# Performance work log

Measured on AMD Instinct MI355X. Metric: run time of the kernel, lower is better.

## Reference

```python
import jax, jax.numpy as jnp
import numpy as np
import math

N_EXP = 8
TOP_K = 2
CAPACITY_FACTOR = 1.25


def _capacity(num_tokens):
    cap = math.floor(TOP_K * CAPACITY_FACTOR * num_tokens / N_EXP)
    cap += cap % 2  # round up to even, as in nanoMoE
    return int(cap)


def setup_inputs() -> dict:
    key = jax.random.key(0)
    k1, k2, k3, k4 = jax.random.split(key, 4)
    B, C, d = 4, 1024, 1024
    x = jax.random.normal(k1, (B, C, d), dtype=jnp.float32)
    w_g = jax.random.normal(k2, (d, N_EXP), dtype=jnp.float32) * 0.02
    c_fc = jax.random.normal(k3, (N_EXP, d, 4 * d), dtype=jnp.float32) * 0.02
    c_proj = jax.random.normal(k4, (N_EXP, 4 * d, d), dtype=jnp.float32) * 0.02
    return {"x": x, "w_g": w_g, "c_fc": c_fc, "c_proj": c_proj}


def reference(x, w_g, c_fc, c_proj):
    B, C, d = x.shape
    T = B * C  # num_tokens (static)
    cap = _capacity(T)
    xt = x.reshape(T, d)

    # ---- Router (no noise: use_noisy_top_k=False, eval) ----
    logits = xt @ w_g                                   # [T, n_exp]
    top_v, top_i = jax.lax.top_k(logits, TOP_K)         # [T, k]
    full = jnp.full_like(logits, -jnp.inf)
    full = full.at[jnp.arange(T)[:, None], top_i].set(top_v)
    probs = jax.nn.softmax(full, axis=-1)               # [T, n_exp]

    # expert assignment mask and intra-expert rank (capacity dropping)
    exp_mask = jax.nn.one_hot(top_i, N_EXP, dtype=jnp.int32)       # [T, k, n_exp]
    exp_mask = jnp.transpose(exp_mask, (1, 0, 2))                  # [k, T, n_exp]
    exp_rank = jnp.cumsum(exp_mask.reshape(TOP_K * T, N_EXP), axis=0) - 1
    exp_rank = exp_rank.reshape(TOP_K, T, N_EXP)
    exp_mask = exp_mask * (exp_rank < cap).astype(jnp.int32)       # drop overflow
    exp_rank = jnp.sum(exp_mask * exp_rank, axis=-1)               # [k, T] slot id

    exp_weights = exp_mask.astype(x.dtype) * probs[None]           # [k, T, n_exp]
    rank_oh = jax.nn.one_hot(exp_rank, cap, dtype=x.dtype)         # [k, T, cap]
    # dense combine weights [T, n_exp, cap] (as in original code)
    cb_weight = jnp.einsum('kte,ktc->tec', exp_weights, rank_oh)
    sec_mask = (cb_weight != 0).astype(x.dtype)                    # dispatch mask

    # dispatch tokens into per-expert batches [n_exp, cap, d]
    exp_batches = jnp.einsum('tec,td->ecd', sec_mask, xt)

    # ---- MLPExperts: batched GEMM -> GELU (exact) -> batched GEMM ----
    h = jax.nn.gelu(jnp.einsum('ecd,edf->ecf', exp_batches, c_fc), approximate=False)
    exp_out = jnp.einsum('ecf,efd->ecd', h, c_proj)                # [n_exp, cap, d]

    # ---- weighted combine: [T, n_exp*cap] @ [n_exp*cap, d] ----
    out = cb_weight.reshape(T, N_EXP * cap) @ exp_out.reshape(N_EXP * cap, d)
    return out.reshape(B, C, d)
```

## Files before the change

### kernel.cpp

```cpp
#include <hip/hip_runtime.h>
#include <hip/hip_bf16.h>
#include <math.h>

#define T_TOK 4096
#define D     1024
#define DFF   4096
#define NEXP  8
#define CAP   1280
#define TOPK  2

typedef __bf16 bf16x8 __attribute__((ext_vector_type(8)));
typedef float floatx4 __attribute__((ext_vector_type(4)));

__device__ __forceinline__ unsigned short f2bf(float f) {
  union { float f; unsigned u; } un; un.f = f;
  unsigned r = un.u + 0x7FFF + ((un.u >> 16) & 1);
  return (unsigned short)(r >> 16);
}

__global__ __launch_bounds__(256) void router_kernel(
    const float* __restrict__ x, const float* __restrict__ wg,
    int* __restrict__ top_e, float* __restrict__ top_p) {
  int t = blockIdx.x * 4 + (threadIdx.x >> 6);
  int lane = threadIdx.x & 63;
  if (t >= T_TOK) return;
  const float* xr = x + (size_t)t * D;
  float acc[NEXP];
#pragma unroll
  for (int e = 0; e < NEXP; e++) acc[e] = 0.f;
  for (int dd = lane; dd < D; dd += 64) {
    float xv = xr[dd];
    const float* wr = wg + dd * NEXP;
#pragma unroll
    for (int e = 0; e < NEXP; e++) acc[e] += xv * wr[e];
  }
#pragma unroll
  for (int off = 32; off > 0; off >>= 1) {
#pragma unroll
    for (int e = 0; e < NEXP; e++) acc[e] += __shfl_xor(acc[e], off, 64);
  }
  if (lane == 0) {
    int b0 = 0; float v0 = acc[0];
    for (int e = 1; e < NEXP; e++) if (acc[e] > v0) { v0 = acc[e]; b0 = e; }
    int b1 = -1; float v1 = -INFINITY;
    for (int e = 0; e < NEXP; e++) if (e != b0 && acc[e] > v1) { v1 = acc[e]; b1 = e; }
    float e1 = expf(v1 - v0);
    float s = 1.0f + e1;
    top_e[t * 2 + 0] = b0; top_e[t * 2 + 1] = b1;
    top_p[t * 2 + 0] = 1.0f / s; top_p[t * 2 + 1] = e1 / s;
  }
}

__global__ __launch_bounds__(1024) void rank_kernel(
    const int* __restrict__ top_e, const float* __restrict__ top_p,
    int* __restrict__ slot_token, int* __restrict__ tok_slot,
    float* __restrict__ tok_w) {
  __shared__ int wsum[16][NEXP];
  __shared__ int wscan[16][NEXP];
  int tid = threadIdx.x;
  int lane = tid & 63, w = tid >> 6;

  for (int s = tid; s < NEXP * CAP; s += 1024) slot_token[s] = -1;
  __syncthreads();

  int base[NEXP];
#pragma unroll
  for (int e = 0; e < NEXP; e++) base[e] = 0;

  for (int k = 0; k < TOPK; k++) {
    int cnt[NEXP];
#pragma unroll
    for (int e = 0; e < NEXP; e++) cnt[e] = 0;
    int eloc[4];
#pragma unroll
    for (int i = 0; i < 4; i++) {
      int t = tid * 4 + i;
      int e = top_e[t * 2 + k];
      eloc[i] = e;
#pragma unroll
      for (int q = 0; q < NEXP; q++) cnt[q] += (q == e);
    }
    int inc[NEXP];
#pragma unroll
    for (int e = 0; e < NEXP; e++) inc[e] = cnt[e];
    for (int off = 1; off < 64; off <<= 1) {
#pragma unroll
      for (int e = 0; e < NEXP; e++) {
        int v = __shfl_up(inc[e], off, 64);
        if (lane >= off) inc[e] += v;
      }
    }
    if (lane == 63)
#pragma unroll
      for (int e = 0; e < NEXP; e++) wsum[w][e] = inc[e];
    __syncthreads();
    if (w == 0 && lane < 16) {
      int s[NEXP];
#pragma unroll
      for (int e = 0; e < NEXP; e++) s[e] = wsum[lane][e];
      for (int off = 1; off < 16; off <<= 1) {
#pragma unroll
        for (int e = 0; e < NEXP; e++) {
          int v = __shfl_up(s[e], off, 64);
          if (lane >= off) s[e] += v;
        }
      }
#pragma unroll
      for (int e = 0; e < NEXP; e++) wscan[lane][e] = s[e];
    }
    __syncthreads();
    int excl[NEXP];
#pragma unroll
    for (int e = 0; e < NEXP; e++)
      excl[e] = inc[e] - cnt[e] + (w ? wscan[w - 1][e] : 0) + base[e];

    int run[NEXP];
#pragma unroll
    for (int e = 0; e < NEXP; e++) run[e] = 0;
#pragma unroll
    for (int i = 0; i < 4; i++) {
      int t = tid * 4 + i;
      int e = eloc[i];
      int r = 0;
#pragma unroll
      for (int q = 0; q < NEXP; q++)
        if (q == e) { r = excl[q] + run[q]; run[q]++; }
      if (r < CAP) {
        slot_token[e * CAP + r] = t;
        tok_slot[t * 2 + k] = e * CAP + r;
      } else {
        tok_slot[t * 2 + k] = -1;
      }
      tok_w[t * 2 + k] = top_p[t * 2 + k];
    }
#pragma unroll
    for (int e = 0; e < NEXP; e++) base[e] += wscan[15][e];
    __syncthreads();
  }
}

__global__ __launch_bounds__(256) void gather_cvt_kernel(
    const float* __restrict__ x, const int* __restrict__ slot_token,
    unsigned short* __restrict__ xb) {
  int slot = blockIdx.x;
  int tok = slot_token[slot];
  int i = threadIdx.x;
  float4 v = make_float4(0.f, 0.f, 0.f, 0.f);
  if (tok >= 0) v = ((const float4*)(x + (size_t)tok * D))[i];
  ushort4 o;
  o.x = f2bf(v.x); o.y = f2bf(v.y); o.z = f2bf(v.z); o.w = f2bf(v.w);
  ((ushort4*)(xb + (size_t)slot * D))[i] = o;
}

__global__ __launch_bounds__(256) void transpose_cvt_kernel(
    const float* __restrict__ src, unsigned short* __restrict__ dst,
    int R, int Cc) {
  __shared__ float tile[64][65];
  int e = blockIdx.z;
  src += (size_t)e * R * Cc;
  dst += (size_t)e * R * Cc;
  int r0 = blockIdx.y * 64, c0 = blockIdx.x * 64;
  int tr = threadIdx.x >> 4;
  int tc = (threadIdx.x & 15) * 4;
#pragma unroll
  for (int i = 0; i < 64; i += 16) {
    float4 v = *(const float4*)(src + (size_t)(r0 + tr + i) * Cc + c0 + tc);
    tile[tr + i][tc + 0] = v.x;
    tile[tr + i][tc + 1] = v.y;
    tile[tr + i][tc + 2] = v.z;
    tile[tr + i][tc + 3] = v.w;
  }
  __syncthreads();
#pragma unroll
  for (int i = 0; i < 64; i += 16) {
    int c = tr + i, r = tc;
    ushort4 o;
    o.x = f2bf(tile[r + 0][c]);
    o.y = f2bf(tile[r + 1][c]);
    o.z = f2bf(tile[r + 2][c]);
    o.w = f2bf(tile[r + 3][c]);
    *(ushort4*)(dst + (size_t)(c0 + c) * R + r0 + r) = o;
  }
}

template <int MODE>
__global__ __launch_bounds__(512, 2) void gemm8_kernel(
    const unsigned short* __restrict__ A,
    const unsigned short* __restrict__ Bt,
    void* __restrict__ Cv) {
  constexpr int NN   = (MODE == 0) ? DFF : D;
  constexpr int KK   = (MODE == 0) ? D : DFF;
  constexpr int NTN  = NN / 256;
  constexpr int NKT  = KK / 64;
  constexpr int STOT = NKT * 4;
  constexpr int REG  = 256 * 32;

  __shared__ unsigned short As[4 * REG];
  __shared__ unsigned short Bs[4 * REG];

  int e    = blockIdx.x & 7;
  int idx  = blockIdx.x >> 3;
  int row0 = (idx / NTN) * 256;
  int col0 = (idx % NTN) * 256;

  int tid  = threadIdx.x;
  int lane = tid & 63, wave = tid >> 6;
  int wm = wave >> 2, wn = wave & 3;
  int fr = lane & 15, fq = lane >> 4;
  int lanesw = (fq ^ ((fr >> 1) & 3)) * 8;

  int srow  = tid >> 2;
  int lslot = (tid & 3) ^ ((srow >> 1) & 3);
  const unsigned short* asrc =
      A + (size_t)e * CAP * KK + (size_t)(row0 + srow) * KK + lslot * 8;
  const unsigned short* bsrc =
      Bt + (size_t)e * NN * KK + (size_t)(col0 + srow) * KK + lslot * 8;

  floatx4 acc[8][4];
#pragma unroll
  for (int m = 0; m < 8; m++)
#pragma unroll
    for (int n = 0; n < 4; n++) acc[m][n] = (floatx4){0.f, 0.f, 0.f, 0.f};

  auto stage = [&](int s) {
    if (s >= STOT) return;
    int kt = s >> 2, j = s & 3, hh = j >> 1;
    const unsigned short* src = (j & 1) ? bsrc : asrc;
    unsigned short* dst =
        ((j & 1) ? Bs : As) + ((kt & 1) * 2 + hh) * REG + tid * 8;
    size_t go = (size_t)kt * 64 + hh * 32;
    __builtin_amdgcn_global_load_lds(
        (const __attribute__((address_space(1))) unsigned int*)(src + go),
        (__attribute__((address_space(3))) unsigned int*)dst, 16, 0, 0);
    __builtin_amdgcn_global_load_lds(
        (const __attribute__((address_space(1))) unsigned int*)(src + go +
                                                               (size_t)128 * KK),
        (__attribute__((address_space(3))) unsigned int*)(dst + REG / 2), 16, 0,
        0);
  };

#pragma unroll
  for (int s = 0; s < 6; s++) stage(s);

  bf16x8 aq[4], bq[4];

  for (int kt = 0; kt < NKT; kt++) {
    const unsigned short* a0 = As + (kt & 1) * 2 * REG;
    const unsigned short* b0 = Bs + (kt & 1) * 2 * REG;
    const unsigned short* a1 = a0 + REG;
    const unsigned short* b1 = b0 + REG;
    int abase = (wm * 128 + fr) * 32 + lanesw;
    int bbase = (wn * 64 + fr) * 32 + lanesw;

    stage(kt * 4 + 6);
    if (kt == NKT - 1)
      asm volatile("s_waitcnt vmcnt(0)" ::: "memory");
    else
      asm volatile("s_waitcnt vmcnt(6)" ::: "memory");
    __builtin_amdgcn_s_barrier();
    __builtin_amdgcn_sched_barrier(0);
#pragma unroll
    for (int n = 0; n < 4; n++)
      bq[n] = *(const bf16x8*)&b0[bbase + n * 512];
#pragma unroll
    for (int m = 0; m < 4; m++)
      aq[m] = *(const bf16x8*)&a0[abase + m * 512];
    __builtin_amdgcn_s_setprio(1);
#pragma unroll
    for (int m = 0; m < 4; m++)
#pragma unroll
      for (int n = 0; n < 4; n++)
        acc[m][n] = __builtin_amdgcn_mfma_f32_16x16x32_bf16(aq[m], bq[n],
                                                            acc[m][n], 0, 0, 0);
    __builtin_amdgcn_s_setprio(0);
    __builtin_amdgcn_s_barrier();

#pragma unroll
    for (int m = 0; m < 4; m++)
      aq[m] = *(const bf16x8*)&a0[abase + 2048 + m * 512];
    stage(kt * 4 + 7);
    __builtin_amdgcn_s_barrier();
    __builtin_amdgcn_s_setprio(1);
#pragma unroll
    for (int m = 0; m < 4; m++)
#pragma unroll
      for (int n = 0; n < 4; n++)
        acc[4 + m][n] = __builtin_amdgcn_mfma_f32_16x16x32_bf16(
            aq[m], bq[n], acc[4 + m][n], 0, 0, 0);
    __builtin_amdgcn_s_setprio(0);
    __builtin_amdgcn_s_barrier();

#pragma unroll
    for (int n = 0; n < 4; n++)
      bq[n] = *(const bf16x8*)&b1[bbase + n * 512];
#pragma unroll
    for (int m = 0; m < 4; m++)
      aq[m] = *(const bf16x8*)&a1[abase + m * 512];
    stage(kt * 4 + 8);
    __builtin_amdgcn_s_barrier();
    __builtin_amdgcn_s_setprio(1);
#pragma unroll
    for (int m = 0; m < 4; m++)
#pragma unroll
      for (int n = 0; n < 4; n++)
        acc[m][n] = __builtin_amdgcn_mfma_f32_16x16x32_bf16(aq[m], bq[n],
                                                            acc[m][n], 0, 0, 0);
    __builtin_amdgcn_s_setprio(0);
    __builtin_amdgcn_s_barrier();

#pragma unroll
    for (int m = 0; m < 4; m++)
      aq[m] = *(const bf16x8*)&a1[abase + 2048 + m * 512];
    stage(kt * 4 + 9);
    __builtin_amdgcn_s_barrier();
    __builtin_amdgcn_s_setprio(1);
#pragma unroll
    for (int m = 0; m < 4; m++)
#pragma unroll
      for (int n = 0; n < 4; n++)
        acc[4 + m][n] = __builtin_amdgcn_mfma_f32_16x16x32_bf16(
            aq[m], bq[n], acc[4 + m][n], 0, 0, 0);
    __builtin_amdgcn_s_setprio(0);
    __builtin_amdgcn_s_barrier();
  }

  if (MODE == 0) {
    unsigned short* Ce = (unsigned short*)Cv + (size_t)e * CAP * DFF +
                         (size_t)(row0 + wm * 128 + fq * 4) * DFF + col0 +
                         wn * 64 + fr;
#pragma unroll
    for (int m = 0; m < 8; m++)
#pragma unroll
      for (int r = 0; r < 4; r++) {
        size_t ro = (size_t)(m * 16 + r) * DFF;
#pragma unroll
        for (int n = 0; n < 4; n++) {
          float v = acc[m][n][r];
          v = 0.5f * v * (1.f + erff(v * 0.70710678118654752f));
          Ce[ro + n * 16] = f2bf(v);
        }
      }
  } else {
    float* Ce = (float*)Cv + (size_t)e * CAP * D +
                (size_t)(row0 + wm * 128 + fq * 4) * D + col0 + wn * 64 + fr;
#pragma unroll
    for (int m = 0; m < 8; m++)
#pragma unroll
      for (int r = 0; r < 4; r++) {
        size_t ro = (size_t)(m * 16 + r) * D;
#pragma unroll
        for (int n = 0; n < 4; n++) Ce[ro + n * 16] = acc[m][n][r];
      }
  }
}

__global__ __launch_bounds__(256) void combine_kernel(
    const float* __restrict__ eo, const int* __restrict__ tok_slot,
    const float* __restrict__ tok_w, float* __restrict__ out) {
  int t = blockIdx.x;
  int i = threadIdx.x;
  float4 acc = make_float4(0.f, 0.f, 0.f, 0.f);
#pragma unroll
  for (int k = 0; k < TOPK; k++) {
    int s = tok_slot[t * 2 + k];
    if (s >= 0) {
      float w = tok_w[t * 2 + k];
      float4 v = ((const float4*)(eo + (size_t)s * D))[i];
      acc.x += w * v.x;
      acc.y += w * v.y;
      acc.z += w * v.z;
      acc.w += w * v.w;
    }
  }
  ((float4*)(out + (size_t)t * D))[i] = acc;
}

extern "C" void kernel_launch(void* const* d_in, const int* in_sizes, int n_in,
                              void* d_out, int out_size, void* d_ws, size_t ws_size,
                              hipStream_t stream) {
  const float* x     = (const float*)d_in[0];
  const float* wg    = (const float*)d_in[1];
  const float* cfc   = (const float*)d_in[2];
  const float* cproj = (const float*)d_in[3];
  float* out = (float*)d_out;

  char* ws = (char*)d_ws;
  size_t off = 0;
  auto alloc = [&](size_t bytes) -> void* {
    void* p = ws + off;
    off += (bytes + 255) & ~(size_t)255;
    return p;
  };
  int*   top_e      = (int*)  alloc((size_t)T_TOK * 2 * 4);
  float* top_p      = (float*)alloc((size_t)T_TOK * 2 * 4);
  int*   slot_token = (int*)  alloc((size_t)NEXP * CAP * 4);
  int*   tok_slot   = (int*)  alloc((size_t)T_TOK * 2 * 4);
  float* tok_w      = (float*)alloc((size_t)T_TOK * 2 * 4);
  unsigned short* xb      = (unsigned short*)alloc((size_t)NEXP * CAP * D * 2);
  unsigned short* cfc_t   = (unsigned short*)alloc((size_t)NEXP * D * DFF * 2);
  unsigned short* cproj_t = (unsigned short*)alloc((size_t)NEXP * DFF * D * 2);
  unsigned short* h       = (unsigned short*)alloc((size_t)NEXP * CAP * DFF * 2);
  float* eo = (float*)xb;

  transpose_cvt_kernel<<<dim3(DFF / 64, D / 64, NEXP), 256, 0, stream>>>(
      cfc, cfc_t, D, DFF);
  transpose_cvt_kernel<<<dim3(D / 64, DFF / 64, NEXP), 256, 0, stream>>>(
      cproj, cproj_t, DFF, D);

  router_kernel<<<T_TOK / 4, 256, 0, stream>>>(x, wg, top_e, top_p);
  rank_kernel<<<1, 1024, 0, stream>>>(top_e, top_p, slot_token, tok_slot, tok_w);
  gather_cvt_kernel<<<NEXP * CAP, 256, 0, stream>>>(x, slot_token, xb);

  gemm8_kernel<0><<<NEXP * (CAP / 256) * (DFF / 256), 512, 0, stream>>>(
      xb, cfc_t, h);
  gemm8_kernel<1><<<NEXP * (CAP / 256) * (D / 256), 512, 0, stream>>>(
      h, cproj_t, eo);

  combine_kernel<<<T_TOK, 256, 0, stream>>>(eo, tok_slot, tok_w, out);
}
```

Measured before the change: 617.2 us.

## Reschedule GEMM LDS reads ahead of barriers and use fast erf GELU

Moves the LDS fragment reads ahead of the stage issue and barrier, so the vmcnt wait happens once per K iteration at the end instead of at the start. Explicit lgkmcnt waits and sched_barriers keep register loads overlapped with in-flight global-to-LDS copies. Also replaces erff in the GELU epilogue with an Abramowitz-Stegun polynomial built on rcp and exp, trading a small accuracy loss for fewer instructions. The waitcnt rework risks race conditions if the counts are wrong.

Result: faster. 604.3 us (-2.1%).

```diff
diff --git a/kernel.cpp b/kernel.cpp
--- a/kernel.cpp
+++ b/kernel.cpp
@@ -16,6 +16,17 @@
   union { float f; unsigned u; } un; un.f = f;
   unsigned r = un.u + 0x7FFF + ((un.u >> 16) & 1);
   return (unsigned short)(r >> 16);
+}
+
+__device__ __forceinline__ float gelu_exact(float v) {
+  float z  = v * 0.70710678118654752f;
+  float az = fabsf(z);
+  float t  = __builtin_amdgcn_rcpf(fmaf(0.3275911f, az, 1.0f));
+  float p  = fmaf(fmaf(fmaf(fmaf(1.061405429f, t, -1.453152027f), t,
+                            1.421413741f), t, -0.284496736f), t, 0.254829592f) * t;
+  float ex = __expf(-z * z);
+  float er = copysignf(fmaf(-p, ex, 1.0f), z);
+  return 0.5f * v * (1.0f + er);
 }
 
 __global__ __launch_bounds__(256) void router_kernel(
@@ -241,6 +252,8 @@
 
 #pragma unroll
   for (int s = 0; s < 6; s++) stage(s);
+  asm volatile("s_waitcnt vmcnt(4)" ::: "memory");
+  __builtin_amdgcn_s_barrier();
 
   bf16x8 aq[4], bq[4];
 
@@ -252,19 +265,15 @@
     int abase = (wm * 128 + fr) * 32 + lanesw;
     int bbase = (wn * 64 + fr) * 32 + lanesw;
 
+#pragma unroll
+    for (int n = 0; n < 4; n++) bq[n] = *(const bf16x8*)&b0[bbase + n * 512];
+#pragma unroll
+    for (int m = 0; m < 4; m++) aq[m] = *(const bf16x8*)&a0[abase + m * 512];
     stage(kt * 4 + 6);
-    if (kt == NKT - 1)
-      asm volatile("s_waitcnt vmcnt(0)" ::: "memory");
-    else
-      asm volatile("s_waitcnt vmcnt(6)" ::: "memory");
-    __builtin_amdgcn_s_barrier();
-    __builtin_amdgcn_sched_barrier(0);
-#pragma unroll
-    for (int n = 0; n < 4; n++)
-      bq[n] = *(const bf16x8*)&b0[bbase + n * 512];
-#pragma unroll
-    for (int m = 0; m < 4; m++)
-      aq[m] = *(const bf16x8*)&a0[abase + m * 512];
+    __builtin_amdgcn_sched_barrier(0);
+    __builtin_amdgcn_s_barrier();
+    asm volatile("s_waitcnt lgkmcnt(0)" ::: "memory");
+    __builtin_amdgcn_sched_barrier(0);
     __builtin_amdgcn_s_setprio(1);
 #pragma unroll
     for (int m = 0; m < 4; m++)
@@ -279,7 +288,10 @@
     for (int m = 0; m < 4; m++)
       aq[m] = *(const bf16x8*)&a0[abase + 2048 + m * 512];
     stage(kt * 4 + 7);
-    __builtin_amdgcn_s_barrier();
+    __builtin_amdgcn_sched_barrier(0);
+    __builtin_amdgcn_s_barrier();
+    asm volatile("s_waitcnt lgkmcnt(0)" ::: "memory");
+    __builtin_amdgcn_sched_barrier(0);
     __builtin_amdgcn_s_setprio(1);
 #pragma unroll
     for (int m = 0; m < 4; m++)
@@ -291,13 +303,14 @@
     __builtin_amdgcn_s_barrier();
 
 #pragma unroll
-    for (int n = 0; n < 4; n++)
-      bq[n] = *(const bf16x8*)&b1[bbase + n * 512];
-#pragma unroll
-    for (int m = 0; m < 4; m++)
-      aq[m] = *(const bf16x8*)&a1[abase + m * 512];
+    for (int n = 0; n < 4; n++) bq[n] = *(const bf16x8*)&b1[bbase + n * 512];
+#pragma unroll
+    for (int m = 0; m < 4; m++) aq[m] = *(const bf16x8*)&a1[abase + m * 512];
     stage(kt * 4 + 8);
-    __builtin_amdgcn_s_barrier();
+    __builtin_amdgcn_sched_barrier(0);
+    __builtin_amdgcn_s_barrier();
+    asm volatile("s_waitcnt lgkmcnt(0)" ::: "memory");
+    __builtin_amdgcn_sched_barrier(0);
     __builtin_amdgcn_s_setprio(1);
 #pragma unroll
     for (int m = 0; m < 4; m++)
@@ -312,7 +325,14 @@
     for (int m = 0; m < 4; m++)
       aq[m] = *(const bf16x8*)&a1[abase + 2048 + m * 512];
     stage(kt * 4 + 9);
-    __builtin_amdgcn_s_barrier();
+    if (kt >= NKT - 2)
+      asm volatile("s_waitcnt vmcnt(0)" ::: "memory");
+    else
+      asm volatile("s_waitcnt vmcnt(4)" ::: "memory");
+    __builtin_amdgcn_sched_barrier(0);
+    __builtin_amdgcn_s_barrier();
+    asm volatile("s_waitcnt lgkmcnt(0)" ::: "memory");
+    __builtin_amdgcn_sched_barrier(0);
     __builtin_amdgcn_s_setprio(1);
 #pragma unroll
     for (int m = 0; m < 4; m++)
@@ -334,11 +354,8 @@
       for (int r = 0; r < 4; r++) {
         size_t ro = (size_t)(m * 16 + r) * DFF;
 #pragma unroll
-        for (int n = 0; n < 4; n++) {
-          float v = acc[m][n][r];
-          v = 0.5f * v * (1.f + erff(v * 0.70710678118654752f));
-          Ce[ro + n * 16] = f2bf(v);
-        }
+        for (int n = 0; n < 4; n++)
+          Ce[ro + n * 16] = f2bf(gelu_exact(acc[m][n][r]));
       }
   } else {
     float* Ce = (float*)Cv + (size_t)e * CAP * D +
```
